# Optimization experiments

Measured on AMD Instinct MI355X. Metric: run time of the kernel, lower is better.

The kernel has to match this reference:

```python
import jax, jax.numpy as jnp
import numpy as np

N_NODES = 100000
NUM_FEATURES = 64
HIDDEN = 128
OUT_CONV2 = 100


def gcn_conv(x, W, b, src, dst, n):
    """PyG GCNConv: add self-loops, symmetric degree norm, scatter-add."""
    x = x @ W  # [N, out]
    loop = jnp.arange(n, dtype=src.dtype)
    src2 = jnp.concatenate([src, loop])  # [E+N]
    dst2 = jnp.concatenate([dst, loop])
    deg = jax.ops.segment_sum(jnp.ones_like(dst2, dtype=x.dtype), dst2, num_segments=n)
    dinv = jnp.where(deg > 0, deg ** -0.5, 0.0)
    norm = dinv[src2] * dinv[dst2]  # [E+N]
    msg = x[src2] * norm[:, None]  # gather + scale
    out = jax.ops.segment_sum(msg, dst2, num_segments=n)  # scatter-add
    return out + b


def setup_inputs() -> dict:
    key = jax.random.key(0)
    ks = jax.random.split(key, 8)
    E = 1600000
    x = jax.random.normal(ks[0], (N_NODES, NUM_FEATURES), dtype=jnp.float32)
    edge_index = jax.random.randint(ks[1], (2, E), 0, N_NODES, dtype=jnp.int64)
    # Glorot-style init for GCNConv weights, zeros bias (PyG defaults)
    s1 = (6.0 / (NUM_FEATURES + HIDDEN)) ** 0.5
    W1 = jax.random.uniform(ks[2], (NUM_FEATURES, HIDDEN), minval=-s1, maxval=s1, dtype=jnp.float32)
    b1 = jnp.zeros((HIDDEN,), dtype=jnp.float32)
    s2 = (6.0 / (HIDDEN + OUT_CONV2)) ** 0.5
    W2 = jax.random.uniform(ks[3], (HIDDEN, OUT_CONV2), minval=-s2, maxval=s2, dtype=jnp.float32)
    b2 = jnp.zeros((OUT_CONV2,), dtype=jnp.float32)
    sl = (1.0 / OUT_CONV2) ** 0.5
    Wl = jax.random.uniform(ks[4], (OUT_CONV2, 1), minval=-sl, maxval=sl, dtype=jnp.float32)
    bl = jax.random.uniform(ks[5], (1,), minval=-sl, maxval=sl, dtype=jnp.float32)
    return {"x": x, "edge_index": edge_index, "W1": W1, "b1": b1,
            "W2": W2, "b2": b2, "Wl": Wl, "bl": bl}


def reference(x, edge_index, W1, b1, W2, b2, Wl, bl):
    src, dst = edge_index[0], edge_index[1]
    h = gcn_conv(x, W1, b1, src, dst, N_NODES)
    h = jax.nn.relu(h)
    # F.dropout with training=False (eval/inference) is identity
    h = gcn_conv(h, W2, b2, src, dst, N_NODES)
    return h @ Wl + bl  # [N, 1]
```

## Files before the change

### kernel.cpp

```cpp
#include <hip/hip_runtime.h>
#include <hip/hip_fp16.h>


#define N_NODES 100000
#define F_IN 64
#define HID 128
#define OUT2 100
#define BSHIFT 7
#define BNODES 128
#define NBUCKETS ((N_NODES + BNODES - 1) / BNODES)
#define SCAP 2560
#define ACHUNK 4096
#define NB_PAD 1024
#define SENTB 0xFFFFu
#define SENTE 0xFFFFFFFFu
#define TSHIFT 13
#define NTILES 13
#define RSTRIDE 72
#define ZROW N_NODES
#define YSCALE 4096.0f
#define YINV   (1.0f / 4096.0f)
#define ZSCALE 8192.0f
#define ZINV   (1.0f / 8192.0f)

typedef _Float16 half8 __attribute__((ext_vector_type(8)));
typedef float f32x4 __attribute__((ext_vector_type(4)));

static __device__ __forceinline__ half8 as_half8(uint4 u) {
    union { uint4 u; half8 h; } x; x.u = u; return x.h;
}

__global__ __launch_bounds__(256) void partA_kernel(
    const int* __restrict__ src, const int* __restrict__ dst,
    int* __restrict__ bcur, unsigned int* __restrict__ ebuf, int E, int nchunks,
    const float* __restrict__ W1, const float* __restrict__ W2,
    const float* __restrict__ b2, const float* __restrict__ Wl,
    const float* __restrict__ bl,
    float* __restrict__ v, float* __restrict__ c, uint4* __restrict__ Wpk,
    int* __restrict__ yzero) {
    int t = threadIdx.x;
    if ((int)blockIdx.x >= nchunks) {
        int pb = (int)blockIdx.x - nchunks;
        if (pb < 8) {
            int idx = pb * 256 + t;
            int lane2 = idx & 63;
            int kf    = (idx >> 6) & 1;
            int cb    = (idx >> 7) & 7;
            int part  = (idx >> 10) & 1;
            union { uint4 u; unsigned short s[8]; } pk;
            #pragma unroll
            for (int j = 0; j < 8; ++j) {
                int k    = kf * 32 + (lane2 >> 4) * 8 + j;
                int colg = cb * 16 + (lane2 & 15);
                float w = W1[k * HID + colg];
                __half h = __float2half_rn(w);
                if (part) h = __float2half_rn(w - __half2float(h));
                pk.s[j] = __half_as_ushort(h);
            }
            Wpk[idx] = pk.u;
        } else {
            if (t < HID) {
                float acc = 0.f;
                for (int k = 0; k < OUT2; ++k) acc += W2[t * OUT2 + k] * Wl[k];
                v[t] = acc;
            } else if (t == HID) {
                float acc = bl[0];
                for (int k = 0; k < OUT2; ++k) acc += b2[k] * Wl[k];
                *c = acc;
            }
            if (t < 128) yzero[t] = 0;
        }
        return;
    }
    __shared__ unsigned int stage[ACHUNK];
    __shared__ unsigned short sb[ACHUNK];
    __shared__ int hist[NB_PAD];
    __shared__ int ocnt[NB_PAD];
    __shared__ int gbase[NB_PAD];
    __shared__ int cnt2[NB_PAD];
    __shared__ int tsum[256];
    int base = blockIdx.x * ACHUNK;
    int total = E - base; if (total > ACHUNK) total = ACHUNK;

    #pragma unroll
    for (int i = 0; i < 4; ++i) { hist[t + i * 256] = 0; cnt2[t + i * 256] = 0; }
    __syncthreads();

    unsigned int pe[16];
    unsigned short bk[16];
    #pragma unroll
    for (int k = 0; k < 16; ++k) {
        int e = base + k * 256 + t;
        if (e < E) {
            int s = src[e], d = dst[e];
            pe[k] = ((unsigned int)s << BSHIFT) | (unsigned int)(d & (BNODES - 1));
            bk[k] = (unsigned short)(d >> BSHIFT);
            atomicAdd(&hist[bk[k]], 1);
        } else {
            bk[k] = SENTB;
        }
    }
    __syncthreads();
    #pragma unroll
    for (int i = 0; i < 4; ++i) ocnt[t + i * 256] = hist[t + i * 256];
    __syncthreads();
    int lcl[4];
    int s = 0;
    #pragma unroll
    for (int i = 0; i < 4; ++i) { s += hist[4 * t + i]; lcl[i] = s; }
    tsum[t] = s;
    __syncthreads();
    for (int off = 1; off < 256; off <<= 1) {
        int vv = (t >= off) ? tsum[t - off] : 0;
        __syncthreads();
        tsum[t] += vv;
        __syncthreads();
    }
    int cbase = tsum[t] - s;
    #pragma unroll
    for (int i = 0; i < 4; ++i) hist[4 * t + i] = cbase + lcl[i];
    __syncthreads();
    #pragma unroll
    for (int i = 0; i < 4; ++i) {
        int b = (t + i * 256 + blockIdx.x * 131) & (NB_PAD - 1);
        int cc = ocnt[b];
        if (cc > 0 && b < NBUCKETS)
            gbase[b] = b * SCAP + atomicAdd(&bcur[b], cc);
    }
    __syncthreads();
    #pragma unroll
    for (int k = 0; k < 16; ++k) {
        if (bk[k] != SENTB) {
            int b = bk[k];
            int pos = (hist[b] - ocnt[b]) + atomicAdd(&cnt2[b], 1);
            stage[pos] = pe[k];
            sb[pos] = (unsigned short)b;
        }
    }
    __syncthreads();
    #pragma unroll
    for (int k = 0; k < 16; ++k) {
        int idx = k * 256 + t;
        if (idx < total) {
            int b = sb[idx];
            int lo = hist[b] - ocnt[b];
            ebuf[gbase[b] + (idx - lo)] = stage[idx];
        }
    }
}

__global__ __launch_bounds__(256) void partB_kernel(
    const int* __restrict__ bcur, unsigned int* __restrict__ csr,
    float* __restrict__ dinv,
    const float4* __restrict__ x4, uint2* __restrict__ y2, int n) {
    __shared__ int lcnt[BNODES];
    __shared__ float sdinv[BNODES];
    __shared__ int tcnt[16];
    __shared__ int tcur[16];
    __shared__ unsigned int sbuf[SCAP];
    int b = blockIdx.x, t = threadIdx.x;
    int node0 = b << BSHIFT;
    int nlocal = min(BNODES, n - node0);
    int base = b * SCAP;
    int cnt = bcur[b];
    if (t < BNODES) lcnt[t] = 0;
    if (t < 16) tcnt[t] = 0;
    __syncthreads();
    unsigned int er[SCAP / 256];
    #pragma unroll
    for (int k = 0; k < SCAP / 256; ++k) {
        int idx = k * 256 + t;
        er[k] = (idx < cnt) ? csr[base + idx] : SENTE;
        if (er[k] != SENTE) {
            atomicAdd(&lcnt[er[k] & (BNODES - 1)], 1);
            atomicAdd(&tcnt[er[k] >> (BSHIFT + TSHIFT)], 1);
        }
    }
    __syncthreads();
    if (t < BNODES) {
        float sd = rsqrtf((float)lcnt[t] + 1.0f);
        sdinv[t] = sd;
        if (t < nlocal) dinv[node0 + t] = sd;
    }
    if (t == 0) {
        int s = 0;
        #pragma unroll
        for (int i = 0; i < NTILES; ++i) { tcur[i] = s; s += tcnt[i]; }
    }
    __syncthreads();
    #pragma unroll
    for (int k = 0; k < SCAP / 256; ++k) {
        unsigned int e = er[k];
        if (e != SENTE) {
            int p = atomicAdd(&tcur[e >> (BSHIFT + TSHIFT)], 1);
            sbuf[p] = e;
        }
    }
    __syncthreads();
    for (int idx = t; idx < cnt; idx += 256) csr[base + idx] = sbuf[idx];
    for (int i = t; i < nlocal * 16; i += 256) {
        int nl = i >> 4;
        int gi = (node0 + nl) * 16 + (i & 15);
        float sc = sdinv[nl] * YSCALE;
        float4 xv = x4[gi];
        int a0 = __float2int_rn(xv.x * sc);
        int a1 = __float2int_rn(xv.y * sc);
        int a2 = __float2int_rn(xv.z * sc);
        int a3 = __float2int_rn(xv.w * sc);
        uint2 pk;
        pk.x = ((unsigned int)a0 & 0xFFFFu) | ((unsigned int)a1 << 16);
        pk.y = ((unsigned int)a2 & 0xFFFFu) | ((unsigned int)a3 << 16);
        y2[gi] = pk;
    }
}

#define F1_ISSUE(EE, U, DL)                                            \
    _Pragma("unroll")                                                  \
    for (int g = 0; g < 8; ++g) {                                      \
        unsigned int e_ = __shfl((EE), g * 8 + q, 64);                 \
        int srow_ = (e_ != SENTE) ? (int)(e_ >> BSHIFT) : ZROW;        \
        DL[g] = (int)(e_ & (BNODES - 1));                              \
        U[g] = y4[srow_ * 8 + col];                                    \
    }

#define F1_CONSUME(U, DL)                                              \
    _Pragma("unroll")                                                  \
    for (int g = 0; g < 8; ++g) {                                      \
        int* rowp_ = &acci[DL[g] * RSTRIDE + col * 9];                 \
        const int* up_ = (const int*)&U[g];                            \
        _Pragma("unroll")                                              \
        for (int j = 0; j < 4; ++j) {                                  \
            int d_ = up_[j];                                           \
            atomicAdd(&rowp_[2 * j],     (d_ << 16) >> 16);            \
            atomicAdd(&rowp_[2 * j + 1], d_ >> 16);                    \
        }                                                              \
    }

__global__ __launch_bounds__(256, 4) void fused1_kernel(
    const int4* __restrict__ y4, const short* __restrict__ yh,
    const unsigned int* __restrict__ csr, const int* __restrict__ bcur,
    const float* __restrict__ dinv, const uint4* __restrict__ Wpk,
    const float* __restrict__ b1, const float* __restrict__ v,
    float* __restrict__ zz, int n) {
    __shared__ int acci[BNODES * RSTRIDE];
    int t = threadIdx.x;
    int lane = t & 63, wave = t >> 6;
    int q = lane >> 3, col = lane & 7;
    int b = blockIdx.x;
    int node0 = b << BSHIFT;
    int nlocal = min(BNODES, n - node0);
    int base = b * SCAP;
    int cnt = bcur[b];

    for (int r = wave; r < BNODES; r += 4) {
        int vv = 0;
        if (r < nlocal) vv = (int)yh[(node0 + r) * 64 + lane];
        acci[r * RSTRIDE + q * 9 + col] = vv;
    }
    __syncthreads();

    int nr = (cnt + 255) >> 8;
    int lpos = wave * 64 + lane;
    unsigned int ee = (lpos < cnt) ? csr[base + lpos] : SENTE;
    for (int r = 0; r < nr; ++r) {
        int pn = lpos + (r + 1) * 256;
        unsigned int een = (pn < cnt) ? csr[base + pn] : SENTE;
        int4 u[8]; int dl[8];
        F1_ISSUE(ee, u, dl);
        __builtin_amdgcn_sched_barrier(0);
        F1_CONSUME(u, dl);
        ee = een;
        __syncthreads();
    }
    __syncthreads();

    int mm = lane & 15, kq = lane >> 4;
    for (int i = 0; i < 2; ++i) {
        int st = wave * 2 + i;
        int row = st * 16 + mm;
        float dis = ((row < nlocal) ? dinv[node0 + row] : 0.f) * YINV;
        const int* ap = &acci[row * RSTRIDE];
        half8 A0, A1;
        #pragma unroll
        for (int j = 0; j < 8; ++j) {
            A0[j] = (_Float16)(dis * (float)ap[kq * 9 + j]);
            A1[j] = (_Float16)(dis * (float)ap[(4 + kq) * 9 + j]);
        }
        f32x4 acc[8];
        #pragma unroll
        for (int cb = 0; cb < 8; ++cb) acc[cb] = (f32x4){0.f, 0.f, 0.f, 0.f};
        #pragma unroll
        for (int cb = 0; cb < 8; ++cb) {
            half8 bh0 = as_half8(Wpk[(cb * 2 + 0) * 64 + lane]);
            half8 bh1 = as_half8(Wpk[(cb * 2 + 1) * 64 + lane]);
            half8 bl0 = as_half8(Wpk[1024 + (cb * 2 + 0) * 64 + lane]);
            half8 bl1 = as_half8(Wpk[1024 + (cb * 2 + 1) * 64 + lane]);
            acc[cb] = __builtin_amdgcn_mfma_f32_16x16x32_f16(A0, bh0, acc[cb], 0, 0, 0);
            acc[cb] = __builtin_amdgcn_mfma_f32_16x16x32_f16(A1, bh1, acc[cb], 0, 0, 0);
            acc[cb] = __builtin_amdgcn_mfma_f32_16x16x32_f16(A0, bl0, acc[cb], 0, 0, 0);
            acc[cb] = __builtin_amdgcn_mfma_f32_16x16x32_f16(A1, bl1, acc[cb], 0, 0, 0);
        }
        float zp[4] = {0.f, 0.f, 0.f, 0.f};
        #pragma unroll
        for (int cb = 0; cb < 8; ++cb) {
            int colg = cb * 16 + mm;
            float bb1 = b1[colg], vv = v[colg];
            #pragma unroll
            for (int rr = 0; rr < 4; ++rr) {
                float h = acc[cb][rr] + bb1;
                h = fmaxf(h, 0.f);
                zp[rr] += h * vv;
            }
        }
        #pragma unroll
        for (int off = 1; off < 16; off <<= 1) {
            #pragma unroll
            for (int rr = 0; rr < 4; ++rr) zp[rr] += __shfl_xor(zp[rr], off, 64);
        }
        if (mm == 0) {
            int nb = st * 16 + kq * 4;
            #pragma unroll
            for (int rr = 0; rr < 4; ++rr)
                if (nb + rr < nlocal)
                    zz[node0 + nb + rr] = dinv[node0 + nb + rr] * zp[rr];
        }
    }
}

__global__ __launch_bounds__(256) void out_kernel(
    const int* __restrict__ bcur, const unsigned int* __restrict__ csr,
    const float* __restrict__ dinv, const float* __restrict__ zz,
    const float* __restrict__ c, float* __restrict__ out, int n) {
    __shared__ int acc2[BNODES];
    int b = blockIdx.x, t = threadIdx.x;
    int node0 = b << BSHIFT;
    int nlocal = min(BNODES, n - node0);
    int base = b * SCAP;
    int cnt = bcur[b];
    if (t < BNODES) acc2[t] = 0;
    __syncthreads();
    for (int idx = t; idx < cnt; idx += 256) {
        unsigned int e = csr[base + idx];
        float z = zz[e >> BSHIFT];
        atomicAdd(&acc2[e & (BNODES - 1)], __float2int_rn(z * ZSCALE));
    }
    __syncthreads();
    if (t < nlocal) {
        int node = node0 + t;
        out[node] = c[0] + dinv[node] * ((float)acc2[t] * ZINV + zz[node]);
    }
}

extern "C" void kernel_launch(void* const* d_in, const int* in_sizes, int n_in,
                              void* d_out, int out_size, void* d_ws, size_t ws_size,
                              hipStream_t stream) {
    const float* x  = (const float*)d_in[0];
    const int*   ei = (const int*)d_in[1];
    const float* W1 = (const float*)d_in[2];
    const float* b1 = (const float*)d_in[3];
    const float* W2 = (const float*)d_in[4];
    const float* b2 = (const float*)d_in[5];
    const float* Wl = (const float*)d_in[6];
    const float* bl = (const float*)d_in[7];
    float* out = (float*)d_out;

    int E = in_sizes[1] / 2;
    const int* src = ei;
    const int* dst = ei + E;

    float* ws      = (float*)d_ws;
    float* dinv    = ws;
    float* zz      = dinv + N_NODES;
    float* v       = zz + N_NODES;
    float* c       = v + HID;
    int*   bcur    = (int*)(c + 4);
    int*   csr     = bcur + NB_PAD;
    uint4* Wpk     = (uint4*)(csr + (size_t)NBUCKETS * SCAP);
    short* y       = (short*)((float*)Wpk + 8192);

    int nchunks = (E + ACHUNK - 1) / ACHUNK;

    hipMemsetAsync(bcur, 0, NBUCKETS * sizeof(int), stream);
    partA_kernel<<<nchunks + 9, 256, 0, stream>>>(
        src, dst, bcur, (unsigned int*)csr, E, nchunks,
        W1, W2, b2, Wl, bl, v, c, Wpk, (int*)(y + (size_t)ZROW * 64));
    partB_kernel<<<NBUCKETS, 256, 0, stream>>>(
        bcur, (unsigned int*)csr, dinv, (const float4*)x, (uint2*)y, N_NODES);
    fused1_kernel<<<NBUCKETS, 256, 0, stream>>>(
        (const int4*)y, (const short*)y, (const unsigned int*)csr,
        bcur, dinv, Wpk, b1, v, zz, N_NODES);
    out_kernel<<<NBUCKETS, 256, 0, stream>>>(
        bcur, (const unsigned int*)csr, dinv, zz, c, out, N_NODES);
}
```

Measured before the change: 176.4 us.

## Compute degrees via global atomics and move tile sort into fused aggregation kernel

Node in-degrees are now counted with global atomics during edge bucketing, so a simple grid-stride kernel can compute dinv and quantize x without reading the CSR buckets. The per-bucket tile sort moves from the old partB kernel into fused1, which sorts edges into shared memory and streams them from LDS. This removes the per-row __syncthreads and the CSR write-back. In exchange it adds 1.6M global atomics in partA, raises fused1's shared memory use and lowers its occupancy bound from 4 to 3 blocks, and clamps bucket counts to SCAP.

Result: slower. 243.3 us (+37.9%).

```diff
diff --git a/kernel.cpp b/kernel.cpp
--- a/kernel.cpp
+++ b/kernel.cpp
@@ -32,7 +32,8 @@
 
 __global__ __launch_bounds__(256) void partA_kernel(
     const int* __restrict__ src, const int* __restrict__ dst,
-    int* __restrict__ bcur, unsigned int* __restrict__ ebuf, int E, int nchunks,
+    int* __restrict__ bcur, int* __restrict__ deg,
+    unsigned int* __restrict__ ebuf, int E, int nchunks,
     const float* __restrict__ W1, const float* __restrict__ W2,
     const float* __restrict__ b2, const float* __restrict__ Wl,
     const float* __restrict__ bl,
@@ -96,6 +97,7 @@
             pe[k] = ((unsigned int)s << BSHIFT) | (unsigned int)(d & (BNODES - 1));
             bk[k] = (unsigned short)(d >> BSHIFT);
             atomicAdd(&hist[bk[k]], 1);
+            atomicAdd(&deg[d], 1);
         } else {
             bk[k] = SENTB;
         }
@@ -149,60 +151,16 @@
     }
 }
 
-__global__ __launch_bounds__(256) void partB_kernel(
-    const int* __restrict__ bcur, unsigned int* __restrict__ csr,
-    float* __restrict__ dinv,
+__global__ __launch_bounds__(256) void y_kernel(
+    const int* __restrict__ deg, float* __restrict__ dinv,
     const float4* __restrict__ x4, uint2* __restrict__ y2, int n) {
-    __shared__ int lcnt[BNODES];
-    __shared__ float sdinv[BNODES];
-    __shared__ int tcnt[16];
-    __shared__ int tcur[16];
-    __shared__ unsigned int sbuf[SCAP];
-    int b = blockIdx.x, t = threadIdx.x;
-    int node0 = b << BSHIFT;
-    int nlocal = min(BNODES, n - node0);
-    int base = b * SCAP;
-    int cnt = bcur[b];
-    if (t < BNODES) lcnt[t] = 0;
-    if (t < 16) tcnt[t] = 0;
-    __syncthreads();
-    unsigned int er[SCAP / 256];
-    #pragma unroll
-    for (int k = 0; k < SCAP / 256; ++k) {
-        int idx = k * 256 + t;
-        er[k] = (idx < cnt) ? csr[base + idx] : SENTE;
-        if (er[k] != SENTE) {
-            atomicAdd(&lcnt[er[k] & (BNODES - 1)], 1);
-            atomicAdd(&tcnt[er[k] >> (BSHIFT + TSHIFT)], 1);
-        }
-    }
-    __syncthreads();
-    if (t < BNODES) {
-        float sd = rsqrtf((float)lcnt[t] + 1.0f);
-        sdinv[t] = sd;
-        if (t < nlocal) dinv[node0 + t] = sd;
-    }
-    if (t == 0) {
-        int s = 0;
-        #pragma unroll
-        for (int i = 0; i < NTILES; ++i) { tcur[i] = s; s += tcnt[i]; }
-    }
-    __syncthreads();
-    #pragma unroll
-    for (int k = 0; k < SCAP / 256; ++k) {
-        unsigned int e = er[k];
-        if (e != SENTE) {
-            int p = atomicAdd(&tcur[e >> (BSHIFT + TSHIFT)], 1);
-            sbuf[p] = e;
-        }
-    }
-    __syncthreads();
-    for (int idx = t; idx < cnt; idx += 256) csr[base + idx] = sbuf[idx];
-    for (int i = t; i < nlocal * 16; i += 256) {
-        int nl = i >> 4;
-        int gi = (node0 + nl) * 16 + (i & 15);
-        float sc = sdinv[nl] * YSCALE;
-        float4 xv = x4[gi];
+    int stride = gridDim.x * blockDim.x;
+    for (int i = blockIdx.x * blockDim.x + threadIdx.x; i < n * 16; i += stride) {
+        int node = i >> 4;
+        float sd = rsqrtf((float)deg[node] + 1.0f);
+        if ((i & 15) == 0) dinv[node] = sd;
+        float sc = sd * YSCALE;
+        float4 xv = x4[i];
         int a0 = __float2int_rn(xv.x * sc);
         int a1 = __float2int_rn(xv.y * sc);
         int a2 = __float2int_rn(xv.z * sc);
@@ -210,7 +168,7 @@
         uint2 pk;
         pk.x = ((unsigned int)a0 & 0xFFFFu) | ((unsigned int)a1 << 16);
         pk.y = ((unsigned int)a2 & 0xFFFFu) | ((unsigned int)a3 << 16);
-        y2[gi] = pk;
+        y2[i] = pk;
     }
 }
 
@@ -236,13 +194,16 @@
         }                                                              \
     }
 
-__global__ __launch_bounds__(256, 4) void fused1_kernel(
+__global__ __launch_bounds__(256, 3) void fused1_kernel(
     const int4* __restrict__ y4, const short* __restrict__ yh,
     const unsigned int* __restrict__ csr, const int* __restrict__ bcur,
     const float* __restrict__ dinv, const uint4* __restrict__ Wpk,
     const float* __restrict__ b1, const float* __restrict__ v,
     float* __restrict__ zz, int n) {
+    __shared__ unsigned int sbuf[SCAP];
     __shared__ int acci[BNODES * RSTRIDE];
+    __shared__ int tcnt[16];
+    __shared__ int tcur[16];
     int t = threadIdx.x;
     int lane = t & 63, wave = t >> 6;
     int q = lane >> 3, col = lane & 7;
@@ -251,26 +212,49 @@
     int nlocal = min(BNODES, n - node0);
     int base = b * SCAP;
     int cnt = bcur[b];
-
+    if (cnt > SCAP) cnt = SCAP;
+
+    if (t < 16) tcnt[t] = 0;
+    __syncthreads();
+
+    unsigned int er[SCAP / 256];
+    #pragma unroll
+    for (int k = 0; k < SCAP / 256; ++k) {
+        int idx = k * 256 + t;
+        er[k] = (idx < cnt) ? csr[base + idx] : SENTE;
+        if (er[k] != SENTE) atomicAdd(&tcnt[er[k] >> (BSHIFT + TSHIFT)], 1);
+    }
     for (int r = wave; r < BNODES; r += 4) {
         int vv = 0;
         if (r < nlocal) vv = (int)yh[(node0 + r) * 64 + lane];
         acci[r * RSTRIDE + q * 9 + col] = vv;
     }
     __syncthreads();
+    if (t == 0) {
+        int s = 0;
+        #pragma unroll
+        for (int i = 0; i < NTILES; ++i) { tcur[i] = s; s += tcnt[i]; }
+    }
+    __syncthreads();
+    #pragma unroll
+    for (int k = 0; k < SCAP / 256; ++k) {
+        unsigned int e = er[k];
+        if (e != SENTE) {
+            int p = atomicAdd(&tcur[e >> (BSHIFT + TSHIFT)], 1);
+            sbuf[p] = e;
+        }
+    }
+    __syncthreads();
 
     int nr = (cnt + 255) >> 8;
     int lpos = wave * 64 + lane;
-    unsigned int ee = (lpos < cnt) ? csr[base + lpos] : SENTE;
     for (int r = 0; r < nr; ++r) {
-        int pn = lpos + (r + 1) * 256;
-        unsigned int een = (pn < cnt) ? csr[base + pn] : SENTE;
+        int p = lpos + r * 256;
+        unsigned int ee = (p < cnt) ? sbuf[p] : SENTE;
         int4 u[8]; int dl[8];
         F1_ISSUE(ee, u, dl);
         __builtin_amdgcn_sched_barrier(0);
         F1_CONSUME(u, dl);
-        ee = een;
-        __syncthreads();
     }
     __syncthreads();
 
@@ -337,6 +321,7 @@
     int nlocal = min(BNODES, n - node0);
     int base = b * SCAP;
     int cnt = bcur[b];
+    if (cnt > SCAP) cnt = SCAP;
     if (t < BNODES) acc2[t] = 0;
     __syncthreads();
     for (int idx = t; idx < cnt; idx += 256) {
@@ -369,23 +354,24 @@
     const int* dst = ei + E;
 
     float* ws      = (float*)d_ws;
-    float* dinv    = ws;
+    int*   deg     = (int*)ws;
+    int*   bcur    = deg + N_NODES;
+    float* dinv    = (float*)(bcur + NB_PAD);
     float* zz      = dinv + N_NODES;
     float* v       = zz + N_NODES;
     float* c       = v + HID;
-    int*   bcur    = (int*)(c + 4);
-    int*   csr     = bcur + NB_PAD;
+    int*   csr     = (int*)(c + 4);
     uint4* Wpk     = (uint4*)(csr + (size_t)NBUCKETS * SCAP);
     short* y       = (short*)((float*)Wpk + 8192);
 
     int nchunks = (E + ACHUNK - 1) / ACHUNK;
 
-    hipMemsetAsync(bcur, 0, NBUCKETS * sizeof(int), stream);
+    hipMemsetAsync(deg, 0, (N_NODES + NB_PAD) * sizeof(int), stream);
     partA_kernel<<<nchunks + 9, 256, 0, stream>>>(
-        src, dst, bcur, (unsigned int*)csr, E, nchunks,
+        src, dst, bcur, deg, (unsigned int*)csr, E, nchunks,
         W1, W2, b2, Wl, bl, v, c, Wpk, (int*)(y + (size_t)ZROW * 64));
-    partB_kernel<<<NBUCKETS, 256, 0, stream>>>(
-        bcur, (unsigned int*)csr, dinv, (const float4*)x, (uint2*)y, N_NODES);
+    y_kernel<<<2048, 256, 0, stream>>>(
+        deg, dinv, (const float4*)x, (uint2*)y, N_NODES);
     fused1_kernel<<<NBUCKETS, 256, 0, stream>>>(
         (const int4*)y, (const short*)y, (const unsigned int*)csr,
         bcur, dinv, Wpk, b1, v, zz, N_NODES);
```

## Simplify edge bucketing and move tile sort into fused aggregation kernel

Applied to the files above, without the earlier changes.

The edge partition kernel drops its shared-memory staging and prefix scan; each edge now gets its rank from a per-bucket atomic and is written straight to global memory, with smaller chunks. The per-bucket source-tile sort moves from partB into fused1, which sorts into shared memory and reads edges from there, so the sorted CSR no longer makes a global write and reread. The per-round __syncthreads in the gather loop is removed, occupancy is lowered to 3 blocks per SM to fit the extra shared buffer, and bucket counts are clamped to SCAP. The risks are scattered, uncoalesced global writes in partA and lower occupancy in fused1.

After: 199.7 us. 1.13x slower.

```diff
diff --git a/kernel.cpp b/kernel.cpp
--- a/kernel.cpp
+++ b/kernel.cpp
@@ -10,12 +10,12 @@
 #define BNODES 128
 #define NBUCKETS ((N_NODES + BNODES - 1) / BNODES)
 #define SCAP 2560
-#define ACHUNK 4096
+#define ACHUNK 2048
 #define NB_PAD 1024
-#define SENTB 0xFFFFu
 #define SENTE 0xFFFFFFFFu
 #define TSHIFT 13
 #define NTILES 13
+#define SCHUNK (SCAP / 256)
 #define RSTRIDE 72
 #define ZROW N_NODES
 #define YSCALE 4096.0f
@@ -72,109 +72,65 @@
         }
         return;
     }
-    __shared__ unsigned int stage[ACHUNK];
-    __shared__ unsigned short sb[ACHUNK];
     __shared__ int hist[NB_PAD];
-    __shared__ int ocnt[NB_PAD];
     __shared__ int gbase[NB_PAD];
     __shared__ int cnt2[NB_PAD];
-    __shared__ int tsum[256];
     int base = blockIdx.x * ACHUNK;
-    int total = E - base; if (total > ACHUNK) total = ACHUNK;
 
     #pragma unroll
     for (int i = 0; i < 4; ++i) { hist[t + i * 256] = 0; cnt2[t + i * 256] = 0; }
     __syncthreads();
 
-    unsigned int pe[16];
-    unsigned short bk[16];
-    #pragma unroll
-    for (int k = 0; k < 16; ++k) {
+    unsigned int pe[8];
+    int bk[8];
+    #pragma unroll
+    for (int k = 0; k < 8; ++k) {
         int e = base + k * 256 + t;
         if (e < E) {
             int s = src[e], d = dst[e];
             pe[k] = ((unsigned int)s << BSHIFT) | (unsigned int)(d & (BNODES - 1));
-            bk[k] = (unsigned short)(d >> BSHIFT);
+            bk[k] = d >> BSHIFT;
             atomicAdd(&hist[bk[k]], 1);
         } else {
-            bk[k] = SENTB;
-        }
-    }
-    __syncthreads();
-    #pragma unroll
-    for (int i = 0; i < 4; ++i) ocnt[t + i * 256] = hist[t + i * 256];
-    __syncthreads();
-    int lcl[4];
-    int s = 0;
-    #pragma unroll
-    for (int i = 0; i < 4; ++i) { s += hist[4 * t + i]; lcl[i] = s; }
-    tsum[t] = s;
-    __syncthreads();
-    for (int off = 1; off < 256; off <<= 1) {
-        int vv = (t >= off) ? tsum[t - off] : 0;
-        __syncthreads();
-        tsum[t] += vv;
-        __syncthreads();
-    }
-    int cbase = tsum[t] - s;
-    #pragma unroll
-    for (int i = 0; i < 4; ++i) hist[4 * t + i] = cbase + lcl[i];
+            bk[k] = -1;
+        }
+    }
     __syncthreads();
     #pragma unroll
     for (int i = 0; i < 4; ++i) {
-        int b = (t + i * 256 + blockIdx.x * 131) & (NB_PAD - 1);
-        int cc = ocnt[b];
+        int b = t + i * 256;
+        int cc = hist[b];
         if (cc > 0 && b < NBUCKETS)
             gbase[b] = b * SCAP + atomicAdd(&bcur[b], cc);
     }
     __syncthreads();
     #pragma unroll
-    for (int k = 0; k < 16; ++k) {
-        if (bk[k] != SENTB) {
+    for (int k = 0; k < 8; ++k) {
+        if (bk[k] >= 0) {
             int b = bk[k];
-            int pos = (hist[b] - ocnt[b]) + atomicAdd(&cnt2[b], 1);
-            stage[pos] = pe[k];
-            sb[pos] = (unsigned short)b;
-        }
-    }
-    __syncthreads();
-    #pragma unroll
-    for (int k = 0; k < 16; ++k) {
-        int idx = k * 256 + t;
-        if (idx < total) {
-            int b = sb[idx];
-            int lo = hist[b] - ocnt[b];
-            ebuf[gbase[b] + (idx - lo)] = stage[idx];
+            int rank = atomicAdd(&cnt2[b], 1);
+            ebuf[gbase[b] + rank] = pe[k];
         }
     }
 }
 
 __global__ __launch_bounds__(256) void partB_kernel(
-    const int* __restrict__ bcur, unsigned int* __restrict__ csr,
+    const int* __restrict__ bcur, const unsigned int* __restrict__ csr,
     float* __restrict__ dinv,
     const float4* __restrict__ x4, uint2* __restrict__ y2, int n) {
     __shared__ int lcnt[BNODES];
     __shared__ float sdinv[BNODES];
-    __shared__ int tcnt[16];
-    __shared__ int tcur[16];
-    __shared__ unsigned int sbuf[SCAP];
     int b = blockIdx.x, t = threadIdx.x;
     int node0 = b << BSHIFT;
     int nlocal = min(BNODES, n - node0);
     int base = b * SCAP;
     int cnt = bcur[b];
+    if (cnt > SCAP) cnt = SCAP;
     if (t < BNODES) lcnt[t] = 0;
-    if (t < 16) tcnt[t] = 0;
-    __syncthreads();
-    unsigned int er[SCAP / 256];
-    #pragma unroll
-    for (int k = 0; k < SCAP / 256; ++k) {
-        int idx = k * 256 + t;
-        er[k] = (idx < cnt) ? csr[base + idx] : SENTE;
-        if (er[k] != SENTE) {
-            atomicAdd(&lcnt[er[k] & (BNODES - 1)], 1);
-            atomicAdd(&tcnt[er[k] >> (BSHIFT + TSHIFT)], 1);
-        }
+    __syncthreads();
+    for (int idx = t; idx < cnt; idx += 256) {
+        unsigned int e = csr[base + idx];
+        atomicAdd(&lcnt[e & (BNODES - 1)], 1);
     }
     __syncthreads();
     if (t < BNODES) {
@@ -182,22 +138,7 @@
         sdinv[t] = sd;
         if (t < nlocal) dinv[node0 + t] = sd;
     }
-    if (t == 0) {
-        int s = 0;
-        #pragma unroll
-        for (int i = 0; i < NTILES; ++i) { tcur[i] = s; s += tcnt[i]; }
-    }
-    __syncthreads();
-    #pragma unroll
-    for (int k = 0; k < SCAP / 256; ++k) {
-        unsigned int e = er[k];
-        if (e != SENTE) {
-            int p = atomicAdd(&tcur[e >> (BSHIFT + TSHIFT)], 1);
-            sbuf[p] = e;
-        }
-    }
-    __syncthreads();
-    for (int idx = t; idx < cnt; idx += 256) csr[base + idx] = sbuf[idx];
+    __syncthreads();
     for (int i = t; i < nlocal * 16; i += 256) {
         int nl = i >> 4;
         int gi = (node0 + nl) * 16 + (i & 15);
@@ -236,13 +177,16 @@
         }                                                              \
     }
 
-__global__ __launch_bounds__(256, 4) void fused1_kernel(
+__global__ __launch_bounds__(256, 3) void fused1_kernel(
     const int4* __restrict__ y4, const short* __restrict__ yh,
     const unsigned int* __restrict__ csr, const int* __restrict__ bcur,
     const float* __restrict__ dinv, const uint4* __restrict__ Wpk,
     const float* __restrict__ b1, const float* __restrict__ v,
     float* __restrict__ zz, int n) {
+    __shared__ unsigned int sbuf[SCAP];
     __shared__ int acci[BNODES * RSTRIDE];
+    __shared__ int tcnt[16];
+    __shared__ int tcur[16];
     int t = threadIdx.x;
     int lane = t & 63, wave = t >> 6;
     int q = lane >> 3, col = lane & 7;
@@ -251,26 +195,49 @@
     int nlocal = min(BNODES, n - node0);
     int base = b * SCAP;
     int cnt = bcur[b];
-
+    if (cnt > SCAP) cnt = SCAP;
+
+    if (t < 16) tcnt[t] = 0;
+    __syncthreads();
+
+    unsigned int er[SCHUNK];
+    #pragma unroll
+    for (int k = 0; k < SCHUNK; ++k) {
+        int idx = k * 256 + t;
+        er[k] = (idx < cnt) ? csr[base + idx] : SENTE;
+        if (er[k] != SENTE) atomicAdd(&tcnt[er[k] >> (BSHIFT + TSHIFT)], 1);
+    }
     for (int r = wave; r < BNODES; r += 4) {
         int vv = 0;
         if (r < nlocal) vv = (int)yh[(node0 + r) * 64 + lane];
         acci[r * RSTRIDE + q * 9 + col] = vv;
     }
     __syncthreads();
+    if (t == 0) {
+        int s = 0;
+        #pragma unroll
+        for (int i = 0; i < NTILES; ++i) { tcur[i] = s; s += tcnt[i]; }
+    }
+    __syncthreads();
+    #pragma unroll
+    for (int k = 0; k < SCHUNK; ++k) {
+        unsigned int e = er[k];
+        if (e != SENTE) {
+            int p = atomicAdd(&tcur[e >> (BSHIFT + TSHIFT)], 1);
+            sbuf[p] = e;
+        }
+    }
+    __syncthreads();
 
     int nr = (cnt + 255) >> 8;
     int lpos = wave * 64 + lane;
-    unsigned int ee = (lpos < cnt) ? csr[base + lpos] : SENTE;
     for (int r = 0; r < nr; ++r) {
-        int pn = lpos + (r + 1) * 256;
-        unsigned int een = (pn < cnt) ? csr[base + pn] : SENTE;
+        int p = lpos + r * 256;
+        unsigned int ee = (p < cnt) ? sbuf[p] : SENTE;
         int4 u[8]; int dl[8];
         F1_ISSUE(ee, u, dl);
         __builtin_amdgcn_sched_barrier(0);
         F1_CONSUME(u, dl);
-        ee = een;
-        __syncthreads();
     }
     __syncthreads();
 
@@ -337,6 +304,7 @@
     int nlocal = min(BNODES, n - node0);
     int base = b * SCAP;
     int cnt = bcur[b];
+    if (cnt > SCAP) cnt = SCAP;
     if (t < BNODES) acc2[t] = 0;
     __syncthreads();
     for (int idx = t; idx < cnt; idx += 256) {
@@ -369,23 +337,23 @@
     const int* dst = ei + E;
 
     float* ws      = (float*)d_ws;
-    float* dinv    = ws;
+    int*   bcur    = (int*)ws;
+    float* dinv    = (float*)(bcur + NB_PAD);
     float* zz      = dinv + N_NODES;
     float* v       = zz + N_NODES;
     float* c       = v + HID;
-    int*   bcur    = (int*)(c + 4);
-    int*   csr     = bcur + NB_PAD;
+    int*   csr     = (int*)(c + 4);
     uint4* Wpk     = (uint4*)(csr + (size_t)NBUCKETS * SCAP);
     short* y       = (short*)((float*)Wpk + 8192);
 
     int nchunks = (E + ACHUNK - 1) / ACHUNK;
 
-    hipMemsetAsync(bcur, 0, NBUCKETS * sizeof(int), stream);
+    hipMemsetAsync(bcur, 0, NB_PAD * sizeof(int), stream);
     partA_kernel<<<nchunks + 9, 256, 0, stream>>>(
         src, dst, bcur, (unsigned int*)csr, E, nchunks,
         W1, W2, b2, Wl, bl, v, c, Wpk, (int*)(y + (size_t)ZROW * 64));
     partB_kernel<<<NBUCKETS, 256, 0, stream>>>(
-        bcur, (unsigned int*)csr, dinv, (const float4*)x, (uint2*)y, N_NODES);
+        bcur, (const unsigned int*)csr, dinv, (const float4*)x, (uint2*)y, N_NODES);
     fused1_kernel<<<NBUCKETS, 256, 0, stream>>>(
         (const int4*)y, (const short*)y, (const unsigned int*)csr,
         bcur, dinv, Wpk, b1, v, zz, N_NODES);
```
